# Kernel tuning notes

Hardware: AMD Instinct MI355X
Metric: run time of the kernel (lower is better)

## Reference

```python
import jax, jax.numpy as jnp
import numpy as np

N_NODES = 100000
N_EDGES = 3200000
STATE_DIM = 128
ACTION_DIM = 8


def _w(key, shape, scale=0.05):
    return (jax.random.normal(key, shape, dtype=jnp.float32) * scale)


def setup_inputs() -> dict:
    key = jax.random.key(0)
    ks = jax.random.split(key, 24)
    x = jax.random.normal(ks[0], (N_NODES, STATE_DIM), dtype=jnp.float32)
    edge_index = jax.random.randint(ks[1], (2, N_EDGES), 0, N_NODES, dtype=jnp.int64)
    inp = {
        "x": x,
        "edge_index": edge_index,
        # GCN layers (weights stored [in, out] so forward is x @ W + b)
        "W1": _w(ks[2], (STATE_DIM, 128)), "b1": jnp.zeros((128,), jnp.float32),
        "W2": _w(ks[3], (128, 128)),       "b2": jnp.zeros((128,), jnp.float32),
        "W3": _w(ks[4], (128, 64)),        "b3": jnp.zeros((64,), jnp.float32),
        # actor MLP 64->128->64->ACTION_DIM + softmax
        "Wa1": _w(ks[5], (64, 128)),  "ba1": jnp.zeros((128,), jnp.float32),
        "Wa2": _w(ks[6], (128, 64)),  "ba2": jnp.zeros((64,), jnp.float32),
        "Wa3": _w(ks[7], (64, ACTION_DIM)), "ba3": jnp.zeros((ACTION_DIM,), jnp.float32),
        # critic MLP 64->128->64->1
        "Wc1": _w(ks[8], (64, 128)),  "bc1": jnp.zeros((128,), jnp.float32),
        "Wc2": _w(ks[9], (128, 64)),  "bc2": jnp.zeros((64,), jnp.float32),
        "Wc3": _w(ks[10], (64, 1)),   "bc3": jnp.zeros((1,), jnp.float32),
    }
    return inp


def _gcn_conv(x, W, b, src, dst, norm):
    # GCNConv: D^{-1/2} (A + I) D^{-1/2} X W + b  (self loops already in src/dst)
    h = x @ W                                   # [N, out]
    msg = h[src] * norm[:, None]                # gather + per-edge scale
    agg = jax.ops.segment_sum(msg, dst, num_segments=N_NODES)
    return agg + b


def reference(x, edge_index,
              W1, b1, W2, b2, W3, b3,
              Wa1, ba1, Wa2, ba2, Wa3, ba3,
              Wc1, bc1, Wc2, bc2, Wc3, bc3):
    loop = jnp.arange(N_NODES, dtype=edge_index.dtype)
    src = jnp.concatenate([edge_index[0], loop])
    dst = jnp.concatenate([edge_index[1], loop])
    deg = jax.ops.segment_sum(jnp.ones_like(dst, dtype=x.dtype), dst,
                              num_segments=N_NODES)
    dinv = jax.lax.rsqrt(deg)                   # deg >= 1 via self loops
    norm = dinv[src] * dinv[dst]                # [E+N]

    # forward_gnn (dropout is identity in eval mode)
    h = jax.nn.relu(_gcn_conv(x, W1, b1, src, dst, norm))
    h = jax.nn.relu(_gcn_conv(h, W2, b2, src, dst, norm))
    h = _gcn_conv(h, W3, b3, src, dst, norm)    # [N, 64]

    a = jax.nn.relu(h @ Wa1 + ba1)
    a = jax.nn.relu(a @ Wa2 + ba2)
    probs = jax.nn.softmax(a @ Wa3 + ba3, axis=-1)   # [N, ACTION_DIM]

    c = jax.nn.relu(h @ Wc1 + bc1)
    c = jax.nn.relu(c @ Wc2 + bc2)
    values = c @ Wc3 + bc3                      # [N, 1]

    return jnp.concatenate([probs, values], axis=-1)  # [N, ACTION_DIM+1]
```

## Files before the change

### kernel.cpp

```cpp
#include <hip/hip_runtime.h>
#include <hip/hip_bf16.h>
#include <math.h>


#define WS_ALIGN(x) (((x) + 255) & ~(size_t)255)

constexpr int RNG  = 64;
constexpr int NRG  = 1563;
constexpr int NB   = 1024;
constexpr int CHK  = 16;

constexpr float S_FP8     = 64.0f;
constexpr float S_FP8_INV = 1.0f / 64.0f;

using bf16x8 = __attribute__((ext_vector_type(8))) short;
using f32x4  = __attribute__((ext_vector_type(4))) float;
using f32x2  = __attribute__((ext_vector_type(2))) float;

__device__ __forceinline__ float b2f(unsigned short u) {
    return __uint_as_float(((unsigned int)u) << 16);
}
__device__ __forceinline__ unsigned short f2b(float f) {
    __hip_bfloat16 hb = __float2bfloat16(f);
    return *(unsigned short*)&hb;
}
__device__ __forceinline__ unsigned char f2fp8(float f) {
    return (unsigned char)(__builtin_amdgcn_cvt_pk_fp8_f32(f, f, 0, false) & 0xff);
}
__device__ __forceinline__ int pad8(int v) { return (v + 7) & ~7; }

__device__ __forceinline__ void acc8(uint2 u, f32x2& a01, f32x2& a23,
                                     f32x2& a45, f32x2& a67) {
    a01 += __builtin_amdgcn_cvt_pk_f32_fp8((int)u.x, false);
    a23 += __builtin_amdgcn_cvt_pk_f32_fp8((int)u.x, true);
    a45 += __builtin_amdgcn_cvt_pk_f32_fp8((int)u.y, false);
    a67 += __builtin_amdgcn_cvt_pk_f32_fp8((int)u.y, true);
}


__global__ __launch_bounds__(256) void bucket_count_k(
    const int* __restrict__ dst, int* __restrict__ bcnt, int E) {
    __shared__ int c64[RNG];
    int b = blockIdx.x, t = threadIdx.x;
    if (t < RNG) c64[t] = 0;
    __syncthreads();
    int ec = (E + NB - 1) / NB;
    int e0 = b * ec, e1 = min(E, e0 + ec);
    for (int e = e0 + t; e < e1; e += 256) {
        int d = __builtin_nontemporal_load(dst + e);
        atomicAdd(&c64[d / NRG], 1);
    }
    __syncthreads();
    if (t < RNG) bcnt[t * NB + b] = c64[t];
}

__global__ __launch_bounds__(256) void rsum_k(
    const int* __restrict__ bcnt, int* __restrict__ base, int* __restrict__ rtot) {
    __shared__ int s[256];
    int r = blockIdx.x, t = threadIdx.x;
    const int* row = bcnt + (size_t)r * NB;
    int v[4], loc = 0;
#pragma unroll
    for (int j = 0; j < 4; j++) { v[j] = row[t * 4 + j]; loc += v[j]; }
    s[t] = loc;
    __syncthreads();
    for (int d = 1; d < 256; d <<= 1) {
        int x = (t >= d) ? s[t - d] : 0;
        __syncthreads();
        s[t] += x;
        __syncthreads();
    }
    int run = s[t] - loc;
    int* bp = base + (size_t)r * NB + t * 4;
#pragma unroll
    for (int j = 0; j < 4; j++) { bp[j] = run; run += v[j]; }
    if (t == 255) rtot[r] = s[255];
}

__global__ void rstart_k(const int* __restrict__ rtot, int* __restrict__ bstart) {
    if (threadIdx.x == 0) {
        int run = 0;
        for (int r = 0; r < RNG; r++) { bstart[r] = run; run += rtot[r]; }
        bstart[RNG] = run;
    }
}

__global__ __launch_bounds__(256) void bucket_scatter_k(
    const int* __restrict__ src, const int* __restrict__ dst,
    const int* __restrict__ base, const int* __restrict__ bstart,
    unsigned* __restrict__ bucket, int E) {
    __shared__ int cur[RNG];
    int b = blockIdx.x, t = threadIdx.x;
    if (t < RNG) cur[t] = bstart[t] + base[(size_t)t * NB + b];
    __syncthreads();
    int ec = (E + NB - 1) / NB;
    int e0 = b * ec, e1 = min(E, e0 + ec);
    for (int e = e0 + t; e < e1; e += 256) {
        int d = __builtin_nontemporal_load(dst + e);
        int sv = __builtin_nontemporal_load(src + e);
        int r = d / NRG;
        int pos = atomicAdd(&cur[r], 1);
        bucket[pos] = ((unsigned)(d - r * NRG) << 17) | (unsigned)sv;
    }
}

__global__ __launch_bounds__(256) void hist_bucket_k(
    const unsigned* __restrict__ bucket, const int* __restrict__ bstart,
    int* __restrict__ hist) {
    __shared__ int h[NRG];
    int b = blockIdx.x, r = b & 63, c2 = b >> 6, t = threadIdx.x;
    for (int i = t; i < NRG; i += 256) h[i] = 0;
    int s0 = bstart[r], s1 = bstart[r + 1];
    int ec = (s1 - s0 + CHK - 1) / CHK;
    int e0 = s0 + c2 * ec, e1 = min(s1, e0 + ec);
    __syncthreads();
    for (int e = e0 + t; e < e1; e += 256) {
        unsigned v = __builtin_nontemporal_load(bucket + e);
        atomicAdd(&h[v >> 17], 1);
    }
    __syncthreads();
    int* out = hist + ((size_t)r * CHK + c2) * NRG;
    for (int i = t; i < NRG; i += 256) out[i] = h[i];
}

__global__ void sum_hist_dinv_k(const int* __restrict__ hist, int* __restrict__ cnt,
                                float* __restrict__ dinv, int N) {
    int i = blockIdx.x * 256 + threadIdx.x;
    if (i >= N) return;
    int r = i / NRG, li = i - r * NRG;
    const int* hp = hist + ((size_t)r * CHK) * NRG + li;
    int s = 0;
#pragma unroll
    for (int c = 0; c < CHK; c++) s += hp[(size_t)c * NRG];
    cnt[i] = s;
    dinv[i] = rsqrtf((float)s + 1.0f);
}

__global__ void chunk_sum_k(const int* __restrict__ cnt, int* __restrict__ bsum, int n) {
    __shared__ int sd[256];
    int t = threadIdx.x;
    int i = blockIdx.x * 256 + t;
    sd[t] = (i < n) ? pad8(cnt[i]) : 0;
    __syncthreads();
    for (int d = 128; d > 0; d >>= 1) {
        if (t < d) sd[t] += sd[t + d];
        __syncthreads();
    }
    if (t == 0) bsum[blockIdx.x] = sd[0];
}

__global__ void scan_mid_k(const int* __restrict__ bsum, int* __restrict__ boff,
                           int nb, int* __restrict__ rowptr, int N) {
    __shared__ int s[512];
    int t = threadIdx.x;
    s[t] = (t < nb) ? bsum[t] : 0;
    __syncthreads();
    if (t == 0) {
        int run = 0;
        for (int i = 0; i < nb; i++) { int v = s[i]; s[i] = run; run += v; }
        rowptr[N] = run;
    }
    __syncthreads();
    if (t < nb) boff[t] = s[t];
}

__global__ void scan_final_k(const int* __restrict__ cnt, const int* __restrict__ boff,
                             int* __restrict__ rowptr, int n) {
    __shared__ int s[256];
    int t = threadIdx.x;
    int i = blockIdx.x * 256 + t;
    int v = (i < n) ? pad8(cnt[i]) : 0;
    s[t] = v;
    __syncthreads();
    for (int d = 1; d < 256; d <<= 1) {
        int x = (t >= d) ? s[t - d] : 0;
        __syncthreads();
        s[t] += x;
        __syncthreads();
    }
    if (i < n) rowptr[i] = s[t] - v + boff[blockIdx.x];
}

__global__ void offsets_k(int* __restrict__ hist, const int* __restrict__ rowptr, int N) {
    int i = blockIdx.x * 256 + threadIdx.x;
    if (i >= N) return;
    int r = i / NRG, li = i - r * NRG;
    int* hp = hist + ((size_t)r * CHK) * NRG + li;
    int run = rowptr[i];
#pragma unroll
    for (int c = 0; c < CHK; c++) {
        int v = hp[(size_t)c * NRG];
        hp[(size_t)c * NRG] = run;
        run += v;
    }
}

__global__ __launch_bounds__(256) void fill2_k(
    const unsigned* __restrict__ bucket, const int* __restrict__ bstart,
    const int* __restrict__ hist, int* __restrict__ col) {
    __shared__ int cur[NRG];
    int b = blockIdx.x, r = b & 63, c2 = b >> 6, t = threadIdx.x;
    const int* hp = hist + ((size_t)r * CHK + c2) * NRG;
    for (int i = t; i < NRG; i += 256) cur[i] = hp[i];
    int s0 = bstart[r], s1 = bstart[r + 1];
    int ec = (s1 - s0 + CHK - 1) / CHK;
    int e0 = s0 + c2 * ec, e1 = min(s1, e0 + ec);
    __syncthreads();
    for (int e = e0 + t; e < e1; e += 256) {
        unsigned v = __builtin_nontemporal_load(bucket + e);
        int slot = atomicAdd(&cur[v >> 17], 1);
        col[slot] = (int)(v & 0x1FFFFu);
    }
}

__global__ void pad_col_k(const int* __restrict__ cnt, const int* __restrict__ rowptr,
                          int* __restrict__ col, int N) {
    int i = blockIdx.x * 256 + threadIdx.x;
    if (i >= N) return;
    int e = rowptr[i] + cnt[i], end = rowptr[i + 1];
    for (; e < end; e++) col[e] = N;
}


__global__ __launch_bounds__(256) void prep_w_k(
    const float* __restrict__ W1, const float* __restrict__ W2,
    const float* __restrict__ W3, const float* __restrict__ Wa1,
    const float* __restrict__ Wa2, const float* __restrict__ Wc1,
    const float* __restrict__ Wc2, unsigned short* __restrict__ wt) {
    int i = blockIdx.x * 256 + threadIdx.x;
    const float* W; int off, K, OUT;
    if (i < 16384)      { W = W1;  off = 0;     K = 128; OUT = 128; }
    else if (i < 32768) { W = W2;  off = 16384; K = 128; OUT = 128; }
    else if (i < 40960) { W = W3;  off = 32768; K = 128; OUT = 64; }
    else if (i < 49152) { W = Wa1; off = 40960; K = 64;  OUT = 128; }
    else if (i < 57344) { W = Wa2; off = 49152; K = 128; OUT = 64; }
    else if (i < 65536) { W = Wc1; off = 57344; K = 64;  OUT = 128; }
    else                { W = Wc2; off = 65536; K = 128; OUT = 64; }
    int j = i - off, k = j / OUT, n = j - k * OUT;
    wt[off + n * K + k] = f2b(W[j]);
}


template <int K, int OUT, bool AF32, bool BIAS_RELU, bool OFP8>
__global__ __launch_bounds__(256) void gemm_mfma_k(
    const void* __restrict__ Xv, const unsigned short* __restrict__ Wt,
    const float* __restrict__ sb,
    void* __restrict__ Yv, int N) {
    constexpr int LDK = K + 8;
    __shared__ __align__(16) unsigned short As[64 * LDK];
    __shared__ __align__(16) unsigned short Bs[OUT * LDK];
    int t = threadIdx.x;
    int rowBase = blockIdx.x * 64;

    if constexpr (AF32) {
        const float* X = (const float*)Xv;
        for (int g = t; g < 64 * (K / 8); g += 256) {
            int r = g / (K / 8), q = g - r * (K / 8);
            int gr = rowBase + r;
            unsigned short us[8];
            if (gr < N) {
                float4 v0 = *(const float4*)(X + (size_t)gr * K + q * 8);
                float4 v1 = *(const float4*)(X + (size_t)gr * K + q * 8 + 4);
                us[0] = f2b(v0.x); us[1] = f2b(v0.y); us[2] = f2b(v0.z); us[3] = f2b(v0.w);
                us[4] = f2b(v1.x); us[5] = f2b(v1.y); us[6] = f2b(v1.z); us[7] = f2b(v1.w);
            } else {
#pragma unroll
                for (int j = 0; j < 8; j++) us[j] = 0;
            }
            *(uint4*)&As[r * LDK + q * 8] = *(uint4*)us;
        }
    } else {
        const unsigned short* X = (const unsigned short*)Xv;
        for (int g = t; g < 64 * (K / 8); g += 256) {
            int r = g / (K / 8), q = g - r * (K / 8);
            int gr = rowBase + r;
            uint4 v = make_uint4(0, 0, 0, 0);
            if (gr < N) v = *(const uint4*)(X + (size_t)gr * K + q * 8);
            *(uint4*)&As[r * LDK + q * 8] = v;
        }
    }
    for (int g = t; g < OUT * (K / 8); g += 256) {
        int r = g / (K / 8), q = g - r * (K / 8);
        *(uint4*)&Bs[r * LDK + q * 8] = *(const uint4*)(Wt + r * K + q * 8);
    }
    __syncthreads();

    int wv = t >> 6, lane = t & 63;
    int lm = lane & 15, lq = lane >> 4;
    constexpr int CT = OUT / 16;
    f32x4 acc[CT];
#pragma unroll
    for (int c = 0; c < CT; c++) acc[c] = (f32x4){0.f, 0.f, 0.f, 0.f};

    const unsigned short* arow = &As[(wv * 16 + lm) * LDK + lq * 8];
#pragma unroll
    for (int kt = 0; kt < K / 32; kt++) {
        bf16x8 a = *(const bf16x8*)(arow + kt * 32);
#pragma unroll
        for (int c = 0; c < CT; c++) {
            bf16x8 b = *(const bf16x8*)&Bs[(c * 16 + lm) * LDK + kt * 32 + lq * 8];
            acc[c] = __builtin_amdgcn_mfma_f32_16x16x32_bf16(a, b, acc[c], 0, 0, 0);
        }
    }

    int r0 = rowBase + wv * 16 + lq * 4;
#pragma unroll
    for (int r = 0; r < 4; r++) {
        int gr = r0 + r;
        if constexpr (OFP8) {
            float scale = (gr < N) ? sb[gr] * S_FP8 : 0.f;
#pragma unroll
            for (int c = 0; c < CT; c++) {
                int colg = c * 16 + lm;
                ((unsigned char*)Yv)[(size_t)gr * OUT + colg] = f2fp8(acc[c][r] * scale);
            }
        } else if (gr < N) {
#pragma unroll
            for (int c = 0; c < CT; c++) {
                int colg = c * 16 + lm;
                float v = acc[c][r];
                if constexpr (BIAS_RELU) v = fmaxf(v + sb[colg], 0.f);
                else v = v * sb[gr];
                ((unsigned short*)Yv)[(size_t)gr * OUT + colg] = f2b(v);
            }
        }
    }
}


template <bool RELU>
__global__ __launch_bounds__(256) void agg128_k(
    const unsigned char* __restrict__ H,
    const int* __restrict__ rowptr, const int* __restrict__ col,
    const float* __restrict__ dinv, const float* __restrict__ bias,
    unsigned short* __restrict__ Y, int N, int Ecap) {
    int tid = threadIdx.x;
    int node = blockIdx.x * 4 + (tid >> 6);
    if (node >= N) return;
    int lane = tid & 63;
    int grp = lane >> 4;
    int li8 = (lane & 15) * 8;

    f32x2 a01 = {0.f, 0.f}, a23 = {0.f, 0.f}, a45 = {0.f, 0.f}, a67 = {0.f, 0.f};
    if (grp == 0) {
        uint2 u = *(const uint2*)(H + (size_t)node * 128 + li8);
        acc8(u, a01, a23, a45, a67);
    }

    int start = rowptr[node], end = rowptr[node + 1];
    for (int e0 = start; e0 < end; e0 += 64) {
        int cv = col[min(e0 + lane, Ecap - 1)];
        int quads = min(64, end - e0) >> 2;
        for (int q = 0; q < quads; q += 2) {
            int s0 = __shfl(cv, 4 * q + grp, 64);
            int s1 = __shfl(cv, 4 * q + 4 + grp, 64);
            uint2 u0 = *(const uint2*)(H + (size_t)s0 * 128 + li8);
            uint2 u1 = *(const uint2*)(H + (size_t)s1 * 128 + li8);
            acc8(u0, a01, a23, a45, a67);
            acc8(u1, a01, a23, a45, a67);
        }
    }

#pragma unroll
    for (int w = 16; w < 64; w <<= 1) {
        a01[0] += __shfl_xor(a01[0], w, 64); a01[1] += __shfl_xor(a01[1], w, 64);
        a23[0] += __shfl_xor(a23[0], w, 64); a23[1] += __shfl_xor(a23[1], w, 64);
        a45[0] += __shfl_xor(a45[0], w, 64); a45[1] += __shfl_xor(a45[1], w, 64);
        a67[0] += __shfl_xor(a67[0], w, 64); a67[1] += __shfl_xor(a67[1], w, 64);
    }

    if (grp == 0) {
        float dv = dinv[node] * S_FP8_INV;
        float4 b0 = *(const float4*)(bias + li8);
        float4 b1 = *(const float4*)(bias + li8 + 4);
        float o0 = a01[0] * dv + b0.x, o1 = a01[1] * dv + b0.y;
        float o2 = a23[0] * dv + b0.z, o3 = a23[1] * dv + b0.w;
        float o4 = a45[0] * dv + b1.x, o5 = a45[1] * dv + b1.y;
        float o6 = a67[0] * dv + b1.z, o7 = a67[1] * dv + b1.w;
        if (RELU) {
            o0 = fmaxf(o0, 0.f); o1 = fmaxf(o1, 0.f); o2 = fmaxf(o2, 0.f); o3 = fmaxf(o3, 0.f);
            o4 = fmaxf(o4, 0.f); o5 = fmaxf(o5, 0.f); o6 = fmaxf(o6, 0.f); o7 = fmaxf(o7, 0.f);
        }
        unsigned short us[8] = {f2b(o0), f2b(o1), f2b(o2), f2b(o3),
                                f2b(o4), f2b(o5), f2b(o6), f2b(o7)};
        *(uint4*)(Y + (size_t)node * 128 + li8) = *(uint4*)us;
    }
}

__global__ __launch_bounds__(256) void agg64_k(
    const unsigned char* __restrict__ H,
    const int* __restrict__ rowptr, const int* __restrict__ col,
    const float* __restrict__ dinv, const float* __restrict__ bias,
    unsigned short* __restrict__ Y, int N, int Ecap) {
    int tid = threadIdx.x;
    int node = blockIdx.x * 4 + (tid >> 6);
    if (node >= N) return;
    int lane = tid & 63;
    int grp = lane >> 3;
    int li8 = (lane & 7) * 8;

    f32x2 a01 = {0.f, 0.f}, a23 = {0.f, 0.f}, a45 = {0.f, 0.f}, a67 = {0.f, 0.f};
    if (grp == 0) {
        uint2 u = *(const uint2*)(H + (size_t)node * 64 + li8);
        acc8(u, a01, a23, a45, a67);
    }

    int start = rowptr[node], end = rowptr[node + 1];
    for (int e0 = start; e0 < end; e0 += 64) {
        int cv = col[min(e0 + lane, Ecap - 1)];
        int octs = min(64, end - e0) >> 3;
        int o = 0;
        for (; o + 2 <= octs; o += 2) {
            int s0 = __shfl(cv, 8 * o + grp, 64);
            int s1 = __shfl(cv, 8 * o + 8 + grp, 64);
            uint2 u0 = *(const uint2*)(H + (size_t)s0 * 64 + li8);
            uint2 u1 = *(const uint2*)(H + (size_t)s1 * 64 + li8);
            acc8(u0, a01, a23, a45, a67);
            acc8(u1, a01, a23, a45, a67);
        }
        if (o < octs) {
            int s0 = __shfl(cv, 8 * o + grp, 64);
            uint2 u0 = *(const uint2*)(H + (size_t)s0 * 64 + li8);
            acc8(u0, a01, a23, a45, a67);
        }
    }

#pragma unroll
    for (int w = 8; w < 64; w <<= 1) {
        a01[0] += __shfl_xor(a01[0], w, 64); a01[1] += __shfl_xor(a01[1], w, 64);
        a23[0] += __shfl_xor(a23[0], w, 64); a23[1] += __shfl_xor(a23[1], w, 64);
        a45[0] += __shfl_xor(a45[0], w, 64); a45[1] += __shfl_xor(a45[1], w, 64);
        a67[0] += __shfl_xor(a67[0], w, 64); a67[1] += __shfl_xor(a67[1], w, 64);
    }

    if (grp == 0) {
        float dv = dinv[node] * S_FP8_INV;
        float4 b0 = *(const float4*)(bias + li8);
        float4 b1 = *(const float4*)(bias + li8 + 4);
        unsigned short us[8] = {
            f2b(a01[0] * dv + b0.x), f2b(a01[1] * dv + b0.y),
            f2b(a23[0] * dv + b0.z), f2b(a23[1] * dv + b0.w),
            f2b(a45[0] * dv + b1.x), f2b(a45[1] * dv + b1.y),
            f2b(a67[0] * dv + b1.z), f2b(a67[1] * dv + b1.w)};
        *(uint4*)(Y + (size_t)node * 64 + li8) = *(uint4*)us;
    }
}


__global__ __launch_bounds__(256) void logits_k(
    const unsigned short* __restrict__ A2,
    const unsigned short* __restrict__ C2,
    const float* __restrict__ Wa3, const float* __restrict__ ba3,
    const float* __restrict__ Wc3, const float* __restrict__ bc3,
    float* __restrict__ out, int N) {
    int t = threadIdx.x;
    int node = blockIdx.x * 32 + (t >> 3);
    int a = t & 7;
    if (node >= N) return;

    const unsigned short* ar = A2 + (size_t)node * 64;
    float s = ba3[a];
#pragma unroll
    for (int q = 0; q < 8; q++) {
        uint4 pv = *(const uint4*)(ar + q * 8);
        const unsigned short* pu = (const unsigned short*)&pv;
#pragma unroll
        for (int j = 0; j < 8; j++)
            s = fmaf(b2f(pu[j]), Wa3[(q * 8 + j) * 8 + a], s);
    }
    float m = s;
#pragma unroll
    for (int w = 1; w < 8; w <<= 1) m = fmaxf(m, __shfl_xor(m, w, 64));
    float e = expf(s - m);
    float sum = e;
#pragma unroll
    for (int w = 1; w < 8; w <<= 1) sum += __shfl_xor(sum, w, 64);
    out[(size_t)node * 9 + a] = e / sum;

    if (a == 0) {
        const unsigned short* cr = C2 + (size_t)node * 64;
        float v = bc3[0];
#pragma unroll
        for (int q = 0; q < 8; q++) {
            uint4 pv = *(const uint4*)(cr + q * 8);
            const unsigned short* pu = (const unsigned short*)&pv;
#pragma unroll
            for (int j = 0; j < 8; j++)
                v = fmaf(b2f(pu[j]), Wc3[q * 8 + j], v);
        }
        out[(size_t)node * 9 + 8] = v;
    }
}


extern "C" void kernel_launch(void* const* d_in, const int* in_sizes, int n_in,
                              void* d_out, int out_size, void* d_ws, size_t ws_size,
                              hipStream_t stream) {
    const float* x   = (const float*)d_in[0];
    const int*   ei  = (const int*)d_in[1];
    const float* W1  = (const float*)d_in[2];  const float* b1  = (const float*)d_in[3];
    const float* W2  = (const float*)d_in[4];  const float* b2  = (const float*)d_in[5];
    const float* W3  = (const float*)d_in[6];  const float* b3  = (const float*)d_in[7];
    const float* Wa1 = (const float*)d_in[8];  const float* ba1 = (const float*)d_in[9];
    const float* Wa2 = (const float*)d_in[10]; const float* ba2 = (const float*)d_in[11];
    const float* Wa3 = (const float*)d_in[12]; const float* ba3 = (const float*)d_in[13];
    const float* Wc1 = (const float*)d_in[14]; const float* bc1 = (const float*)d_in[15];
    const float* Wc2 = (const float*)d_in[16]; const float* bc2 = (const float*)d_in[17];
    const float* Wc3 = (const float*)d_in[18]; const float* bc3 = (const float*)d_in[19];
    float* out = (float*)d_out;

    const int N = in_sizes[0] / 128;
    const int E = in_sizes[1] / 2;
    const int* src = ei;
    const int* dst = ei + E;
    const int Ecap = E + 8 * N;
    const int Npad = ((N + 63) / 64) * 64;

    size_t off = 0;
    auto take = [&](size_t bytes) { size_t o = off; off = WS_ALIGN(off + bytes); return o; };
    char* ws = (char*)d_ws;
    unsigned short* h      = (unsigned short*)(ws + take((size_t)N * 128 * 2));
    unsigned char*  hpr8   = (unsigned char*) (ws + take((size_t)(Npad + 64) * 128));
    unsigned short* h3     = (unsigned short*)(ws + take((size_t)N * 64 * 2));
    int*            col    = (int*)(ws + take((size_t)Ecap * 4));
    unsigned short* A1C1   = (unsigned short*)(ws + take((size_t)N * 128 * 2));
    unsigned short* wt     = (unsigned short*)(ws + take(73728 * 2));
    float* dinv   = (float*)(ws + take((size_t)(N + 64) * 4));
    int*   cnt    = (int*)  (ws + take((size_t)N * 4));
    int*   rowptr = (int*)  (ws + take((size_t)(N + 1) * 4));
    int*   bcnt   = (int*)  (ws + take((size_t)RNG * NB * 4));
    int*   base   = (int*)  (ws + take((size_t)RNG * NB * 4));
    int*   rtot   = (int*)  (ws + take(RNG * 4));
    int*   bstart = (int*)  (ws + take((RNG + 1) * 4));
    int*   bsum   = (int*)  (ws + take(512 * 4));
    int*   boff   = (int*)  (ws + take(512 * 4));
    unsigned* bucket = (unsigned*)h;
    int* hist = (int*)A1C1;
    unsigned short* A2 = (unsigned short*)col;
    unsigned short* C2 = (unsigned short*)hpr8;
    (void)ws_size; (void)n_in; (void)out_size;

    const int nb  = (N + 255) / 256;
    const int gN  = (N + 255) / 256;
    const int gT  = (N + 63) / 64;

    prep_w_k<<<288, 256, 0, stream>>>(W1, W2, W3, Wa1, Wa2, Wc1, Wc2, wt);
    const unsigned short* W1t  = wt;
    const unsigned short* W2t  = wt + 16384;
    const unsigned short* W3t  = wt + 32768;
    const unsigned short* Wa1t = wt + 40960;
    const unsigned short* Wa2t = wt + 49152;
    const unsigned short* Wc1t = wt + 57344;
    const unsigned short* Wc2t = wt + 65536;

    bucket_count_k<<<NB, 256, 0, stream>>>(dst, bcnt, E);
    rsum_k<<<RNG, 256, 0, stream>>>(bcnt, base, rtot);
    rstart_k<<<1, 64, 0, stream>>>(rtot, bstart);
    bucket_scatter_k<<<NB, 256, 0, stream>>>(src, dst, base, bstart, bucket, E);
    hist_bucket_k<<<RNG * CHK, 256, 0, stream>>>(bucket, bstart, hist);
    sum_hist_dinv_k<<<gN, 256, 0, stream>>>(hist, cnt, dinv, N);
    chunk_sum_k<<<nb, 256, 0, stream>>>(cnt, bsum, N);
    scan_mid_k<<<1, 512, 0, stream>>>(bsum, boff, nb, rowptr, N);
    scan_final_k<<<nb, 256, 0, stream>>>(cnt, boff, rowptr, N);
    offsets_k<<<gN, 256, 0, stream>>>(hist, rowptr, N);
    fill2_k<<<RNG * CHK, 256, 0, stream>>>(bucket, bstart, hist, col);
    pad_col_k<<<gN, 256, 0, stream>>>(cnt, rowptr, col, N);

    gemm_mfma_k<128, 128, true,  false, true><<<gT, 256, 0, stream>>>(x, W1t, dinv, hpr8, N);
    agg128_k<true><<<(N + 3) / 4, 256, 0, stream>>>(hpr8, rowptr, col, dinv, b1, h, N, Ecap);
    gemm_mfma_k<128, 128, false, false, true><<<gT, 256, 0, stream>>>(h, W2t, dinv, hpr8, N);
    agg128_k<true><<<(N + 3) / 4, 256, 0, stream>>>(hpr8, rowptr, col, dinv, b2, h, N, Ecap);
    gemm_mfma_k<128, 64,  false, false, true><<<gT, 256, 0, stream>>>(h, W3t, dinv, hpr8, N);
    agg64_k<<<(N + 3) / 4, 256, 0, stream>>>(hpr8, rowptr, col, dinv, b3, h3, N, Ecap);

    gemm_mfma_k<64,  128, false, true, false><<<gT, 256, 0, stream>>>(h3, Wa1t, ba1, A1C1, N);
    gemm_mfma_k<128, 64,  false, true, false><<<gT, 256, 0, stream>>>(A1C1, Wa2t, ba2, A2, N);
    gemm_mfma_k<64,  128, false, true, false><<<gT, 256, 0, stream>>>(h3, Wc1t, bc1, A1C1, N);
    gemm_mfma_k<128, 64,  false, true, false><<<gT, 256, 0, stream>>>(A1C1, Wc2t, bc2, C2, N);
    logits_k<<<(N + 31) / 32, 256, 0, stream>>>(A2, C2, Wa3, ba3, Wc3, bc3, out, N);
}
```

Before: 507.0 us.

## Fuse head GEMMs and logits, merge CSR scan kernels, use persistent GEMM grid

Merges scan_final, offsets and pad_col into a single kernel. Concatenates the actor and critic first-layer weights into one 64->256 GEMM and fuses the final small projections (softmax logits and value) into the epilogues of the second-layer GEMMs, which removes the logits kernel and the intermediate A2/C2 buffers. Converts the GEMMs to a persistent grid of 512 blocks that loads the weight tile into LDS once and loops over row tiles. The trade-off is more epilogue work per GEMM, including shuffle reductions, and a fixed grid size that may leave parts of the GPU unevenly loaded.

```diff
diff --git a/kernel.cpp b/kernel.cpp
--- a/kernel.cpp
+++ b/kernel.cpp
@@ -77,7 +77,7 @@
     if (t == 255) rtot[r] = s[255];
 }
 
-__global__ void rstart_k(const int* __restrict__ rtot, int* __restrict__ bstart) {
+__global__ void rstart_k(const int* __restrict__ rtot, int* __restrict__ bstart, int E) {
     if (threadIdx.x == 0) {
         int run = 0;
         for (int r = 0; r < RNG; r++) { bstart[r] = run; run += rtot[r]; }
@@ -164,12 +164,15 @@
     if (t < nb) boff[t] = s[t];
 }
 
-__global__ void scan_final_k(const int* __restrict__ cnt, const int* __restrict__ boff,
-                             int* __restrict__ rowptr, int n) {
+__global__ void scan_off_pad_k(const int* __restrict__ cnt, const int* __restrict__ boff,
+                               int* __restrict__ rowptr, int* __restrict__ hist,
+                               int* __restrict__ col, int N) {
     __shared__ int s[256];
     int t = threadIdx.x;
     int i = blockIdx.x * 256 + t;
-    int v = (i < n) ? pad8(cnt[i]) : 0;
+    int cv = (i < N) ? cnt[i] : 0;
+    int v = pad8(cv);
+    if (i >= N) v = 0;
     s[t] = v;
     __syncthreads();
     for (int d = 1; d < 256; d <<= 1) {
@@ -178,20 +181,19 @@
         s[t] += x;
         __syncthreads();
     }
-    if (i < n) rowptr[i] = s[t] - v + boff[blockIdx.x];
-}
-
-__global__ void offsets_k(int* __restrict__ hist, const int* __restrict__ rowptr, int N) {
-    int i = blockIdx.x * 256 + threadIdx.x;
-    if (i >= N) return;
-    int r = i / NRG, li = i - r * NRG;
-    int* hp = hist + ((size_t)r * CHK) * NRG + li;
-    int run = rowptr[i];
-#pragma unroll
-    for (int c = 0; c < CHK; c++) {
-        int v = hp[(size_t)c * NRG];
-        hp[(size_t)c * NRG] = run;
-        run += v;
+    if (i < N) {
+        int rp = s[t] - v + boff[blockIdx.x];
+        rowptr[i] = rp;
+        int r = i / NRG, li = i - r * NRG;
+        int* hp = hist + ((size_t)r * CHK) * NRG + li;
+        int run = rp;
+#pragma unroll
+        for (int c = 0; c < CHK; c++) {
+            int hv = hp[(size_t)c * NRG];
+            hp[(size_t)c * NRG] = run;
+            run += hv;
+        }
+        for (int e = rp + cv; e < rp + v; e++) col[e] = N;
     }
 }
 
@@ -213,19 +215,11 @@
     }
 }
 
-__global__ void pad_col_k(const int* __restrict__ cnt, const int* __restrict__ rowptr,
-                          int* __restrict__ col, int N) {
-    int i = blockIdx.x * 256 + threadIdx.x;
-    if (i >= N) return;
-    int e = rowptr[i] + cnt[i], end = rowptr[i + 1];
-    for (; e < end; e++) col[e] = N;
-}
-
 
 __global__ __launch_bounds__(256) void prep_w_k(
     const float* __restrict__ W1, const float* __restrict__ W2,
     const float* __restrict__ W3, const float* __restrict__ Wa1,
-    const float* __restrict__ Wa2, const float* __restrict__ Wc1,
+    const float* __restrict__ Wc1, const float* __restrict__ Wa2,
     const float* __restrict__ Wc2, unsigned short* __restrict__ wt) {
     int i = blockIdx.x * 256 + threadIdx.x;
     const float* W; int off, K, OUT;
@@ -233,97 +227,169 @@
     else if (i < 32768) { W = W2;  off = 16384; K = 128; OUT = 128; }
     else if (i < 40960) { W = W3;  off = 32768; K = 128; OUT = 64; }
     else if (i < 49152) { W = Wa1; off = 40960; K = 64;  OUT = 128; }
-    else if (i < 57344) { W = Wa2; off = 49152; K = 128; OUT = 64; }
-    else if (i < 65536) { W = Wc1; off = 57344; K = 64;  OUT = 128; }
+    else if (i < 57344) { W = Wc1; off = 49152; K = 64;  OUT = 128; }
+    else if (i < 65536) { W = Wa2; off = 57344; K = 128; OUT = 64; }
     else                { W = Wc2; off = 65536; K = 128; OUT = 64; }
     int j = i - off, k = j / OUT, n = j - k * OUT;
     wt[off + n * K + k] = f2b(W[j]);
 }
 
 
-template <int K, int OUT, bool AF32, bool BIAS_RELU, bool OFP8>
-__global__ __launch_bounds__(256) void gemm_mfma_k(
-    const void* __restrict__ Xv, const unsigned short* __restrict__ Wt,
-    const float* __restrict__ sb,
-    void* __restrict__ Yv, int N) {
+template <int K, int OUT, int EPI, bool AF32>
+__global__ __launch_bounds__(256) void gemm2_k(
+    const void* __restrict__ Xv, int ldx, const unsigned short* __restrict__ Wt,
+    const float* __restrict__ sb, const float* __restrict__ w3b,
+    const float* __restrict__ b3, void* __restrict__ Yv, int N, int NT) {
     constexpr int LDK = K + 8;
+    __shared__ __align__(16) unsigned short Bs[OUT * LDK];
     __shared__ __align__(16) unsigned short As[64 * LDK];
-    __shared__ __align__(16) unsigned short Bs[OUT * LDK];
     int t = threadIdx.x;
-    int rowBase = blockIdx.x * 64;
-
-    if constexpr (AF32) {
-        const float* X = (const float*)Xv;
-        for (int g = t; g < 64 * (K / 8); g += 256) {
-            int r = g / (K / 8), q = g - r * (K / 8);
-            int gr = rowBase + r;
-            unsigned short us[8];
-            if (gr < N) {
-                float4 v0 = *(const float4*)(X + (size_t)gr * K + q * 8);
-                float4 v1 = *(const float4*)(X + (size_t)gr * K + q * 8 + 4);
-                us[0] = f2b(v0.x); us[1] = f2b(v0.y); us[2] = f2b(v0.z); us[3] = f2b(v0.w);
-                us[4] = f2b(v1.x); us[5] = f2b(v1.y); us[6] = f2b(v1.z); us[7] = f2b(v1.w);
-            } else {
-#pragma unroll
-                for (int j = 0; j < 8; j++) us[j] = 0;
-            }
-            *(uint4*)&As[r * LDK + q * 8] = *(uint4*)us;
-        }
-    } else {
-        const unsigned short* X = (const unsigned short*)Xv;
-        for (int g = t; g < 64 * (K / 8); g += 256) {
-            int r = g / (K / 8), q = g - r * (K / 8);
-            int gr = rowBase + r;
-            uint4 v = make_uint4(0, 0, 0, 0);
-            if (gr < N) v = *(const uint4*)(X + (size_t)gr * K + q * 8);
-            *(uint4*)&As[r * LDK + q * 8] = v;
-        }
-    }
+
     for (int g = t; g < OUT * (K / 8); g += 256) {
         int r = g / (K / 8), q = g - r * (K / 8);
         *(uint4*)&Bs[r * LDK + q * 8] = *(const uint4*)(Wt + r * K + q * 8);
     }
-    __syncthreads();
 
     int wv = t >> 6, lane = t & 63;
     int lm = lane & 15, lq = lane >> 4;
     constexpr int CT = OUT / 16;
-    f32x4 acc[CT];
-#pragma unroll
-    for (int c = 0; c < CT; c++) acc[c] = (f32x4){0.f, 0.f, 0.f, 0.f};
-
-    const unsigned short* arow = &As[(wv * 16 + lm) * LDK + lq * 8];
-#pragma unroll
-    for (int kt = 0; kt < K / 32; kt++) {
-        bf16x8 a = *(const bf16x8*)(arow + kt * 32);
-#pragma unroll
-        for (int c = 0; c < CT; c++) {
-            bf16x8 b = *(const bf16x8*)&Bs[(c * 16 + lm) * LDK + kt * 32 + lq * 8];
-            acc[c] = __builtin_amdgcn_mfma_f32_16x16x32_bf16(a, b, acc[c], 0, 0, 0);
-        }
-    }
-
-    int r0 = rowBase + wv * 16 + lq * 4;
-#pragma unroll
-    for (int r = 0; r < 4; r++) {
-        int gr = r0 + r;
-        if constexpr (OFP8) {
-            float scale = (gr < N) ? sb[gr] * S_FP8 : 0.f;
+
+    for (int tile = blockIdx.x; tile < NT; tile += gridDim.x) {
+        int rowBase = tile * 64;
+
+        if constexpr (AF32) {
+            const float* X = (const float*)Xv;
+            for (int g = t; g < 64 * (K / 8); g += 256) {
+                int r = g / (K / 8), q = g - r * (K / 8);
+                int gr = rowBase + r;
+                unsigned short us[8];
+                if (gr < N) {
+                    float4 v0 = *(const float4*)(X + (size_t)gr * ldx + q * 8);
+                    float4 v1 = *(const float4*)(X + (size_t)gr * ldx + q * 8 + 4);
+                    us[0] = f2b(v0.x); us[1] = f2b(v0.y); us[2] = f2b(v0.z); us[3] = f2b(v0.w);
+                    us[4] = f2b(v1.x); us[5] = f2b(v1.y); us[6] = f2b(v1.z); us[7] = f2b(v1.w);
+                } else {
+#pragma unroll
+                    for (int j = 0; j < 8; j++) us[j] = 0;
+                }
+                *(uint4*)&As[r * LDK + q * 8] = *(uint4*)us;
+            }
+        } else {
+            const unsigned short* X = (const unsigned short*)Xv;
+            for (int g = t; g < 64 * (K / 8); g += 256) {
+                int r = g / (K / 8), q = g - r * (K / 8);
+                int gr = rowBase + r;
+                uint4 v = make_uint4(0, 0, 0, 0);
+                if (gr < N) v = *(const uint4*)(X + (size_t)gr * ldx + q * 8);
+                *(uint4*)&As[r * LDK + q * 8] = v;
+            }
+        }
+        __syncthreads();
+
+        f32x4 acc[CT];
+#pragma unroll
+        for (int c = 0; c < CT; c++) acc[c] = (f32x4){0.f, 0.f, 0.f, 0.f};
+
+        const unsigned short* arow = &As[(wv * 16 + lm) * LDK + lq * 8];
+#pragma unroll
+        for (int kt = 0; kt < K / 32; kt++) {
+            bf16x8 a = *(const bf16x8*)(arow + kt * 32);
+#pragma unroll
+            for (int c = 0; c < CT; c++) {
+                bf16x8 b = *(const bf16x8*)&Bs[(c * 16 + lm) * LDK + kt * 32 + lq * 8];
+                acc[c] = __builtin_amdgcn_mfma_f32_16x16x32_bf16(a, b, acc[c], 0, 0, 0);
+            }
+        }
+
+        int r0 = rowBase + wv * 16 + lq * 4;
+        if constexpr (EPI == 0) {
+#pragma unroll
+            for (int r = 0; r < 4; r++) {
+                int gr = r0 + r;
+                float scale = (gr < N) ? sb[gr] * S_FP8 : 0.f;
+#pragma unroll
+                for (int c = 0; c < CT; c++) {
+                    int colg = c * 16 + lm;
+                    ((unsigned char*)Yv)[(size_t)gr * OUT + colg] = f2fp8(acc[c][r] * scale);
+                }
+            }
+        } else if constexpr (EPI == 1) {
+#pragma unroll
+            for (int r = 0; r < 4; r++) {
+                int gr = r0 + r;
+                if (gr < N) {
+#pragma unroll
+                    for (int c = 0; c < CT; c++) {
+                        int colg = c * 16 + lm;
+                        float bb = (colg < 128) ? sb[colg] : w3b[colg - 128];
+                        float v = fmaxf(acc[c][r] + bb, 0.f);
+                        ((unsigned short*)Yv)[(size_t)gr * OUT + colg] = f2b(v);
+                    }
+                }
+            }
+        } else if constexpr (EPI == 2) {
+            float l[4][8];
+#pragma unroll
+            for (int r = 0; r < 4; r++)
+#pragma unroll
+                for (int a = 0; a < 8; a++) l[r][a] = 0.f;
 #pragma unroll
             for (int c = 0; c < CT; c++) {
                 int colg = c * 16 + lm;
-                ((unsigned char*)Yv)[(size_t)gr * OUT + colg] = f2fp8(acc[c][r] * scale);
-            }
-        } else if (gr < N) {
+#pragma unroll
+                for (int r = 0; r < 4; r++) {
+                    float v = fmaxf(acc[c][r] + sb[colg], 0.f);
+#pragma unroll
+                    for (int a = 0; a < 8; a++)
+                        l[r][a] = fmaf(v, w3b[colg * 8 + a], l[r][a]);
+                }
+            }
+#pragma unroll
+            for (int w = 1; w < 16; w <<= 1)
+#pragma unroll
+                for (int r = 0; r < 4; r++)
+#pragma unroll
+                    for (int a = 0; a < 8; a++)
+                        l[r][a] += __shfl_xor(l[r][a], w, 64);
+            if (lm < 8) {
+#pragma unroll
+                for (int r = 0; r < 4; r++) {
+                    int gr = r0 + r;
+                    if (gr < N) {
+                        float lg[8], m = -1e30f;
+#pragma unroll
+                        for (int a = 0; a < 8; a++) { lg[a] = l[r][a] + b3[a]; m = fmaxf(m, lg[a]); }
+                        float sum = 0.f;
+#pragma unroll
+                        for (int a = 0; a < 8; a++) { lg[a] = expf(lg[a] - m); sum += lg[a]; }
+                        ((float*)Yv)[(size_t)gr * 9 + lm] = lg[lm] / sum;
+                    }
+                }
+            }
+        } else {
+            float lv[4] = {0.f, 0.f, 0.f, 0.f};
 #pragma unroll
             for (int c = 0; c < CT; c++) {
                 int colg = c * 16 + lm;
-                float v = acc[c][r];
-                if constexpr (BIAS_RELU) v = fmaxf(v + sb[colg], 0.f);
-                else v = v * sb[gr];
-                ((unsigned short*)Yv)[(size_t)gr * OUT + colg] = f2b(v);
-            }
-        }
+#pragma unroll
+                for (int r = 0; r < 4; r++) {
+                    float v = fmaxf(acc[c][r] + sb[colg], 0.f);
+                    lv[r] = fmaf(v, w3b[colg], lv[r]);
+                }
+            }
+#pragma unroll
+            for (int w = 1; w < 16; w <<= 1)
+#pragma unroll
+                for (int r = 0; r < 4; r++) lv[r] += __shfl_xor(lv[r], w, 64);
+            if (lm == 0) {
+#pragma unroll
+                for (int r = 0; r < 4; r++) {
+                    int gr = r0 + r;
+                    if (gr < N) ((float*)Yv)[(size_t)gr * 9 + 8] = lv[r] + b3[0];
+                }
+            }
+        }
+        __syncthreads();
     }
 }
 
@@ -443,52 +509,6 @@
             f2b(a45[0] * dv + b1.x), f2b(a45[1] * dv + b1.y),
             f2b(a67[0] * dv + b1.z), f2b(a67[1] * dv + b1.w)};
         *(uint4*)(Y + (size_t)node * 64 + li8) = *(uint4*)us;
-    }
-}
-
-
-__global__ __launch_bounds__(256) void logits_k(
-    const unsigned short* __restrict__ A2,
-    const unsigned short* __restrict__ C2,
-    const float* __restrict__ Wa3, const float* __restrict__ ba3,
-    const float* __restrict__ Wc3, const float* __restrict__ bc3,
-    float* __restrict__ out, int N) {
-    int t = threadIdx.x;
-    int node = blockIdx.x * 32 + (t >> 3);
-    int a = t & 7;
-    if (node >= N) return;
-
-    const unsigned short* ar = A2 + (size_t)node * 64;
-    float s = ba3[a];
-#pragma unroll
-    for (int q = 0; q < 8; q++) {
-        uint4 pv = *(const uint4*)(ar + q * 8);
-        const unsigned short* pu = (const unsigned short*)&pv;
-#pragma unroll
-        for (int j = 0; j < 8; j++)
-            s = fmaf(b2f(pu[j]), Wa3[(q * 8 + j) * 8 + a], s);
-    }
-    float m = s;
-#pragma unroll
-    for (int w = 1; w < 8; w <<= 1) m = fmaxf(m, __shfl_xor(m, w, 64));
-    float e = expf(s - m);
-    float sum = e;
-#pragma unroll
-    for (int w = 1; w < 8; w <<= 1) sum += __shfl_xor(sum, w, 64);
-    out[(size_t)node * 9 + a] = e / sum;
-
-    if (a == 0) {
-        const unsigned short* cr = C2 + (size_t)node * 64;
-        float v = bc3[0];
-#pragma unroll
-        for (int q = 0; q < 8; q++) {
-            uint4 pv = *(const uint4*)(cr + q * 8);
-            const unsigned short* pu = (const unsigned short*)&pv;
-#pragma unroll
-            for (int j = 0; j < 8; j++)
-                v = fmaf(b2f(pu[j]), Wc3[q * 8 + j], v);
-        }
-        out[(size_t)node * 9 + 8] = v;
     }
 }
 
@@ -515,15 +535,15 @@
     const int* dst = ei + E;
     const int Ecap = E + 8 * N;
     const int Npad = ((N + 63) / 64) * 64;
+    const int NT   = (N + 63) / 64;
 
     size_t off = 0;
     auto take = [&](size_t bytes) { size_t o = off; off = WS_ALIGN(off + bytes); return o; };
     char* ws = (char*)d_ws;
+    unsigned short* h3     = (unsigned short*)(ws + take((size_t)N * 64 * 2));
     unsigned short* h      = (unsigned short*)(ws + take((size_t)N * 128 * 2));
     unsigned char*  hpr8   = (unsigned char*) (ws + take((size_t)(Npad + 64) * 128));
-    unsigned short* h3     = (unsigned short*)(ws + take((size_t)N * 64 * 2));
     int*            col    = (int*)(ws + take((size_t)Ecap * 4));
-    unsigned short* A1C1   = (unsigned short*)(ws + take((size_t)N * 128 * 2));
     unsigned short* wt     = (unsigned short*)(ws + take(73728 * 2));
     float* dinv   = (float*)(ws + take((size_t)(N + 64) * 4));
     int*   cnt    = (int*)  (ws + take((size_t)N * 4));
@@ -535,47 +555,47 @@
     int*   bsum   = (int*)  (ws + take(512 * 4));
     int*   boff   = (int*)  (ws + take(512 * 4));
     unsigned* bucket = (unsigned*)h;
-    int* hist = (int*)A1C1;
-    unsigned short* A2 = (unsigned short*)col;
-    unsigned short* C2 = (unsigned short*)hpr8;
+    int* hist = (int*)h3;
+    unsigned short* A1C1 = (unsigned short*)h;
     (void)ws_size; (void)n_in; (void)out_size;
 
     const int nb  = (N + 255) / 256;
     const int gN  = (N + 255) / 256;
-    const int gT  = (N + 63) / 64;
-
-    prep_w_k<<<288, 256, 0, stream>>>(W1, W2, W3, Wa1, Wa2, Wc1, Wc2, wt);
+    const int GG  = 512;
+
+    prep_w_k<<<288, 256, 0, stream>>>(W1, W2, W3, Wa1, Wc1, Wa2, Wc2, wt);
     const unsigned short* W1t  = wt;
     const unsigned short* W2t  = wt + 16384;
     const unsigned short* W3t  = wt + 32768;
-    const unsigned short* Wa1t = wt + 40960;
-    const unsigned short* Wa2t = wt + 49152;
-    const unsigned short* Wc1t = wt + 57344;
+    const unsigned short* Wh1t = wt + 40960;
+    const unsigned short* Wa2t = wt + 57344;
     const unsigned short* Wc2t = wt + 65536;
 
     bucket_count_k<<<NB, 256, 0, stream>>>(dst, bcnt, E);
     rsum_k<<<RNG, 256, 0, stream>>>(bcnt, base, rtot);
-    rstart_k<<<1, 64, 0, stream>>>(rtot, bstart);
+    rstart_k<<<1, 64, 0, stream>>>(rtot, bstart, E);
     bucket_scatter_k<<<NB, 256, 0, stream>>>(src, dst, base, bstart, bucket, E);
     hist_bucket_k<<<RNG * CHK, 256, 0, stream>>>(bucket, bstart, hist);
     sum_hist_dinv_k<<<gN, 256, 0, stream>>>(hist, cnt, dinv, N);
     chunk_sum_k<<<nb, 256, 0, stream>>>(cnt, bsum, N);
     scan_mid_k<<<1, 512, 0, stream>>>(bsum, boff, nb, rowptr, N);
-    scan_final_k<<<nb, 256, 0, stream>>>(cnt, boff, rowptr, N);
-    offsets_k<<<gN, 256, 0, stream>>>(hist, rowptr, N);
+    scan_off_pad_k<<<nb, 256, 0, stream>>>(cnt, boff, rowptr, hist, col, N);
     fill2_k<<<RNG * CHK, 256, 0, stream>>>(bucket, bstart, hist, col);
-    pad_col_k<<<gN, 256, 0, stream>>>(cnt, rowptr, col, N);
-
-    gemm_mfma_k<128, 128, true,  false, true><<<gT, 256, 0, stream>>>(x, W1t, dinv, hpr8, N);
+
+    gemm2_k<128, 128, 0, true><<<GG, 256, 0, stream>>>(
+        x, 128, W1t, dinv, nullptr, nullptr, hpr8, N, NT);
     agg128_k<true><<<(N + 3) / 4, 256, 0, stream>>>(hpr8, rowptr, col, dinv, b1, h, N, Ecap);
-    gemm_mfma_k<128, 128, false, false, true><<<gT, 256, 0, stream>>>(h, W2t, dinv, hpr8, N);
+    gemm2_k<128, 128, 0, false><<<GG, 256, 0, stream>>>(
+        h, 128, W2t, dinv, nullptr, nullptr, hpr8, N, NT);
     agg128_k<true><<<(N + 3) / 4, 256, 0, stream>>>(hpr8, rowptr, col, dinv, b2, h, N, Ecap);
-    gemm_mfma_k<128, 64,  false, false, true><<<gT, 256, 0, stream>>>(h, W3t, dinv, hpr8, N);
+    gemm2_k<128, 64, 0, false><<<GG, 256, 0, stream>>>(
+        h, 128, W3t, dinv, nullptr, nullptr, hpr8, N, NT);
     agg64_k<<<(N + 3) / 4, 256, 0, stream>>>(hpr8, rowptr, col, dinv, b3, h3, N, Ecap);
 
-    gemm_mfma_k<64,  128, false, true, false><<<gT, 256, 0, stream>>>(h3, Wa1t, ba1, A1C1, N);
-    gemm_mfma_k<128, 64,  false, true, false><<<gT, 256, 0, stream>>>(A1C1, Wa2t, ba2, A2, N);
-    gemm_mfma_k<64,  128, false, true, false><<<gT, 256, 0, stream>>>(h3, Wc1t, bc1, A1C1, N);
-    gemm_mfma_k<128, 64,  false, true, false><<<gT, 256, 0, stream>>>(A1C1, Wc2t, bc2, C2, N);
-    logits_k<<<(N + 31) / 32, 256, 0, stream>>>(A2, C2, Wa3, ba3, Wc3, bc3, out, N);
-}
+    gemm2_k<64, 256, 1, false><<<GG, 256, 0, stream>>>(
+        h3, 64, Wh1t, ba1, bc1, nullptr, A1C1, N, NT);
+    gemm2_k<128, 64, 2, false><<<GG, 256, 0, stream>>>(
+        A1C1, 256, Wa2t, ba2, Wa3, ba3, out, N, NT);
+    gemm2_k<128, 64, 3, false><<<GG, 256, 0, stream>>>(
+        A1C1 + 128, 256, Wc2t, bc2, Wc3, bc3, out, N, NT);
+}
```

New measurement: 502.2 us. Within noise of the previous version (-1.0%).
